# Performance work log

Measured on AMD Instinct MI355X. Metric: run time of the kernel, lower is better.

Reference implementation:

```python
import jax, jax.numpy as jnp
import numpy as np

N = 100000      # nodes on each bipartite side
E = 1600000     # edges
D_IN = 128      # input feature dim
H, C = 2, 50    # heads, per-head out channels
B = 64          # graphs in batch
NEG_SLOPE = 0.2 # GATConv leaky_relu slope


def setup_inputs() -> dict:
    key = jax.random.key(0)
    ks = jax.random.split(key, 12)
    glorot = lambda k, shape: (jax.random.uniform(k, shape, jnp.float32, -1.0, 1.0)
                               * jnp.sqrt(6.0 / (shape[0] + shape[-1])))
    return {
        "x_s": jax.random.normal(ks[0], (N, D_IN), jnp.float32),
        "x_t": jax.random.normal(ks[1], (N, D_IN), jnp.float32),
        "edge_index": jax.random.randint(ks[2], (2, E), 0, N, jnp.int64),
        "distances": jax.random.uniform(ks[3], (E,), jnp.float32),
        "x_s_batch": jnp.sort(jax.random.randint(ks[4], (N,), 0, B, jnp.int64)),
        "x_t_batch": jnp.sort(jax.random.randint(ks[5], (N,), 0, B, jnp.int64)),
        "W_src": glorot(ks[6], (D_IN, H * C)),
        "W_dst": glorot(ks[7], (D_IN, H * C)),
        "att_src": glorot(ks[8], (H, C)),
        "att_dst": glorot(ks[9], (H, C)),
        "bias_conv": jnp.zeros((H * C,), jnp.float32),
        "fc_w": glorot(ks[10], (H * C, 1)),
        "fc_b": jnp.zeros((1,), jnp.float32),
    }


def reference(x_s, x_t, edge_index, distances, x_s_batch, x_t_batch,
              W_src, W_dst, att_src, att_dst, bias_conv, fc_w, fc_b):
    src, dst = edge_index[0], edge_index[1]
    # Bipartite GATConv (edge_attr ignored: built with edge_dim=None)
    hs = (x_s @ W_src).reshape(N, H, C)            # [N,H,C]
    ht = (x_t @ W_dst).reshape(N, H, C)
    a_src = jnp.einsum('nhc,hc->nh', hs, att_src)  # [N,H]
    a_dst = jnp.einsum('nhc,hc->nh', ht, att_dst)
    e = jax.nn.leaky_relu(a_src[src] + a_dst[dst], NEG_SLOPE)   # [E,H]
    # segment softmax over edges sharing a target node
    m = jax.ops.segment_max(e, dst, num_segments=N)             # [N,H]
    ex = jnp.exp(e - m[dst])
    denom = jax.ops.segment_sum(ex, dst, num_segments=N)
    alpha = ex / (denom[dst] + 1e-16)                           # [E,H]
    # scatter-aggregate weighted source messages
    msg = alpha[:, :, None] * hs[src]                           # [E,H,C]
    out = jax.ops.segment_sum(msg, dst, num_segments=N)         # [N,H,C]
    out = out.reshape(N, H * C) + bias_conv
    x = jax.nn.relu(out)
    # global mean pool (original uses x_s_batch)
    pooled = jax.ops.segment_sum(x, x_s_batch, num_segments=B)
    counts = jax.ops.segment_sum(jnp.ones((N,), x.dtype), x_s_batch, num_segments=B)
    pooled = pooled / jnp.maximum(counts, 1.0)[:, None]         # [B,H*C]
    y = pooled @ fc_w + fc_b                                    # [B,1]
    return y.squeeze(-1)
```

## Files before the change

kernel.cpp:

```cpp
#include <hip/hip_runtime.h>
#include <math.h>

#define D_IN 128
#define HC 100
#define PW 128
#define CAP 64
#define NEG 0.2f
#define BINSH 8
#define NBIN 391
#define BCAP 4608
#define ACH 4096
#define YSLOT 32

typedef __attribute__((ext_vector_type(8))) short short8;
typedef __attribute__((ext_vector_type(4))) float f32x4;
typedef __attribute__((ext_vector_type(2))) float f32x2;

__device__ __forceinline__ float lrelu(float x){ return x > 0.f ? x : NEG*x; }

__device__ __forceinline__ unsigned short f2bf(float f){
  union { float f; unsigned u; } v; v.f = f;
  unsigned r = v.u + 0x7fffu + ((v.u >> 16) & 1u);
  return (unsigned short)(r >> 16);
}
__device__ __forceinline__ float bflo(unsigned u){
  union { unsigned x; float f; } v; v.x = u << 16; return v.f;
}
__device__ __forceinline__ float bfhi(unsigned u){
  union { unsigned x; float f; } v; v.x = u & 0xffff0000u; return v.f;
}

__global__ __launch_bounds__(256) void k_init(const float* __restrict__ Wd,
    const float* __restrict__ attd, const float* __restrict__ Ws,
    const float* __restrict__ bias, const float* __restrict__ fcw,
    const float* __restrict__ fcb, const int* __restrict__ xsb,
    float* __restrict__ wv, float* __restrict__ bias_p, float* __restrict__ fcwp,
    unsigned short* __restrict__ Wp, float* __restrict__ invb,
    int* __restrict__ bincnt, float* __restrict__ ypart,
    float* __restrict__ y, int N, int B){
  __shared__ int lo[257];
  int t = threadIdx.x;
  if (blockIdx.x == 0){
    int h = t >> 7, k = t & 127;
    float s = 0.f;
    #pragma unroll
    for (int c = 0; c < 50; ++c) s += Wd[k*HC + h*50 + c] * attd[h*50 + c];
    wv[t] = s;
    if (t < 128){
      bool cv = (t < 50) || (t >= 56 && t < 106);
      int c = (t < 50) ? t : t - 6;
      bias_p[t] = cv ? bias[c] : 0.f;
      fcwp[t]   = cv ? fcw[c]  : 0.f;
    }
    if (t < B) y[t] = fcb[0];
    bincnt[t] = 0; bincnt[t + 256] = 0;
    if (t <= B && t < 257){
      int key = t, l = 0, hi = N;
      while (l < hi){ int mid = (l+hi)>>1; if (xsb[mid] < key) l = mid+1; else hi = mid; }
      lo[t] = l;
    }
    __syncthreads();
    if (t < B){
      int c = lo[t+1] - lo[t];
      invb[t] = 1.f / (float)((c > 0) ? c : 1);
    }
  } else if (blockIdx.x == 1){
    for (int idx = t; idx < 1792; idx += 256){
      int ct = idx >> 8, kk = (idx >> 6) & 3, lane = idx & 63;
      int kb = kk*32 + (lane >> 4)*8;
      int c  = ct*16 + (lane & 15);
      #pragma unroll
      for (int j = 0; j < 8; ++j){
        float v = (c < HC) ? Ws[(size_t)(kb + j)*HC + c] : 0.f;
        Wp[idx*8 + j] = f2bf(v);
      }
    }
  } else {
    float4 z = make_float4(0.f,0.f,0.f,0.f);
    float4* yp4 = (float4*)ypart + (size_t)(blockIdx.x - 2)*8192;
    for (int i = t; i < 8192; i += 256) yp4[i] = z;
  }
}

__global__ __launch_bounds__(256) void k_fused(
    const float* __restrict__ x_s, const unsigned short* __restrict__ Wp,
    const float* __restrict__ atts, unsigned short* __restrict__ hsb,
    float* __restrict__ a_src,
    const float* __restrict__ x_t, const float* __restrict__ wv,
    float* __restrict__ a_dst,
    const int* __restrict__ ei, int* __restrict__ bincnt,
    int2* __restrict__ ebuf,
    int N, int E, int Gg, int Ga)
{
  __shared__ __align__(16) unsigned char smem[16384];
  int t = threadIdx.x;
  int bid = blockIdx.x;

  if (bid < Gg){
    unsigned short* hls = (unsigned short*)smem;
    int lane = t & 63, w = t >> 6;
    int qr = lane & 15, qq = lane >> 4;
    int row0 = bid*64;

    for (int i = t; i < 4096; i += 256) ((unsigned*)hls)[i] = 0u;

    int arow = row0 + w*16 + qr;
    bool rv = arow < N;
    short8 afr[4];
    const float* xp = x_s + (size_t)arow*D_IN + qq*8;
    #pragma unroll
    for (int kk = 0; kk < 4; ++kk){
      float4 v0 = make_float4(0.f,0.f,0.f,0.f), v1 = v0;
      if (rv){ v0 = *(const float4*)(xp + kk*32); v1 = *(const float4*)(xp + kk*32 + 4); }
      short8 a;
      a[0]=(short)f2bf(v0.x); a[1]=(short)f2bf(v0.y); a[2]=(short)f2bf(v0.z); a[3]=(short)f2bf(v0.w);
      a[4]=(short)f2bf(v1.x); a[5]=(short)f2bf(v1.y); a[6]=(short)f2bf(v1.z); a[7]=(short)f2bf(v1.w);
      afr[kk] = a;
    }

    f32x4 acc[7];
    #pragma unroll
    for (int ct = 0; ct < 7; ++ct) acc[ct] = (f32x4){0.f,0.f,0.f,0.f};
    #pragma unroll
    for (int kk = 0; kk < 4; ++kk){
      #pragma unroll
      for (int ct = 0; ct < 7; ++ct){
        short8 b = *(const short8*)&Wp[(size_t)((ct*4+kk)*64 + lane)*8];
        acc[ct] = __builtin_amdgcn_mfma_f32_16x16x32_bf16(afr[kk], b, acc[ct], 0, 0, 0);
      }
    }

    float p0[4] = {0,0,0,0}, p1[4] = {0,0,0,0};
    #pragma unroll
    for (int ct = 0; ct < 7; ++ct){
      int c = ct*16 + qr;
      if (c < HC){
        float av = atts[c];
        #pragma unroll
        for (int r = 0; r < 4; ++r){
          float v = acc[ct][r];
          if (c < 50) p0[r] += v*av; else p1[r] += v*av;
        }
      }
    }
    #pragma unroll
    for (int d = 1; d < 16; d <<= 1){
      #pragma unroll
      for (int r = 0; r < 4; ++r){
        p0[r] += __shfl_xor(p0[r], d, 64);
        p1[r] += __shfl_xor(p1[r], d, 64);
      }
    }
    if (qr == 0){
      #pragma unroll
      for (int r = 0; r < 4; ++r){
        int row = row0 + w*16 + qq*4 + r;
        if (row < N){ a_src[row*2] = p0[r]; a_src[row*2+1] = p1[r]; }
      }
    }

    __syncthreads();
    #pragma unroll
    for (int ct = 0; ct < 7; ++ct){
      int c = ct*16 + qr;
      if (c < HC){
        int p = (c < 50) ? c : c + 6;
        #pragma unroll
        for (int r = 0; r < 4; ++r)
          hls[(w*16 + qq*4 + r)*PW + p] = f2bf(acc[ct][r]);
      }
    }
    __syncthreads();
    unsigned* hg = (unsigned*)(hsb + (size_t)row0*PW);
    for (int i = t; i < 4096; i += 256) hg[i] = ((unsigned*)hls)[i];

  } else if (bid < Gg + Ga){
    float* wsh = (float*)smem;
    wsh[t] = wv[t];
    __syncthreads();
    int lane = t & 63;
    int n = (bid - Gg)*4 + (t >> 6);
    if (n >= N) return;
    float2 x2 = *(const float2*)&x_t[(size_t)n*D_IN + lane*2];
    float p0 = x2.x*wsh[lane*2]       + x2.y*wsh[lane*2+1];
    float p1 = x2.x*wsh[128+lane*2]   + x2.y*wsh[128+lane*2+1];
    #pragma unroll
    for (int d = 32; d >= 1; d >>= 1){ p0 += __shfl_xor(p0,d,64); p1 += __shfl_xor(p1,d,64); }
    if (lane == 0){ a_dst[n*2] = p0; a_dst[n*2+1] = p1; }

  } else {
    int* cnt   = (int*)smem;
    int* gbase = (int*)smem + 512;
    int e0 = (bid - Gg - Ga) * ACH;
    cnt[t] = 0; cnt[t + 256] = 0;
    __syncthreads();

    int src[16], dst[16], rank[16];
    #pragma unroll
    for (int j = 0; j < 4; ++j){
      int e = e0 + t*16 + j*4;
      bool in = (e + 4 <= E);
      int4 s4 = in ? *(const int4*)&ei[e]     : make_int4(0,0,0,0);
      int4 d4 = in ? *(const int4*)&ei[E + e] : make_int4(-1,-1,-1,-1);
      src[j*4+0]=s4.x; src[j*4+1]=s4.y; src[j*4+2]=s4.z; src[j*4+3]=s4.w;
      dst[j*4+0]=d4.x; dst[j*4+1]=d4.y; dst[j*4+2]=d4.z; dst[j*4+3]=d4.w;
    }
    #pragma unroll
    for (int j = 0; j < 16; ++j)
      rank[j] = (dst[j] >= 0) ? atomicAdd(&cnt[dst[j] >> BINSH], 1) : -1;
    __syncthreads();
    for (int i = t; i < NBIN; i += 256)
      gbase[i] = (cnt[i] > 0) ? atomicAdd(&bincnt[i], cnt[i]) : 0;
    __syncthreads();
    #pragma unroll
    for (int j = 0; j < 16; ++j){
      if (rank[j] >= 0){
        int b = dst[j] >> BINSH;
        int gp = gbase[b] + rank[j];
        if (gp < BCAP) ebuf[(size_t)b*BCAP + gp] = make_int2(src[j], dst[j]);
      }
    }
  }
}

__global__ __launch_bounds__(1024) void k_binB(const int* __restrict__ bincnt,
    const int2* __restrict__ ebuf, int* __restrict__ cur, int* __restrict__ csrc, int N)
{
  __shared__ int cnt2[256];
  int t = threadIdx.x, b = blockIdx.x;
  if (t < 256) cnt2[t] = 0;
  __syncthreads();
  int nE = bincnt[b]; if (nE > BCAP) nE = BCAP;
  const int2* eb = ebuf + (size_t)b*BCAP;
  for (int i = t; i < nE; i += 1024){
    int2 sd = eb[i];
    int ld = sd.y & 255;
    int p = atomicAdd(&cnt2[ld], 1);
    if (p < CAP) csrc[(size_t)sd.y*CAP + p] = sd.x;
  }
  __syncthreads();
  int n = b*256 + t;
  if (t < 256 && n < N) cur[n] = cnt2[t];
}

__global__ __launch_bounds__(256) void k_agg(const int* __restrict__ cur,
    const int* __restrict__ csrc, const float* __restrict__ a_src,
    const float* __restrict__ a_dst, const unsigned short* __restrict__ hsb,
    const float* __restrict__ bias_p, const float* __restrict__ fcwp,
    const int* __restrict__ xsb, float* __restrict__ ypart, int N)
{
  int t = threadIdx.x;
  int lane = t & 63;
  int w = t >> 6;
  int n = blockIdx.x*4 + w;
  if (n >= N) return;

  int deg = cur[n]; if (deg > CAP) deg = CAP;
  size_t o = (size_t)n * CAP;
  float2 ad = *(const float2*)&a_dst[n*2];

  int sreg = (lane < deg) ? csrc[o + lane] : 0;

  int k = lane & 15, g = lane >> 4;
  bool actv = (k < 14);
  bool hsel = (k >= 7);

#define PREF(vv, e) { int s_ = __shfl(sreg, (e), 64); \
    vv = (actv && (e) < deg) ? *(const uint4*)&hsb[(size_t)s_*PW + k*8] \
                             : make_uint4(0u,0u,0u,0u); }

  uint4 v0, v1, v2, v3;
  PREF(v0, g) PREF(v1, 4+g) PREF(v2, 8+g) PREF(v3, 12+g)

  float e0 = -INFINITY, e1 = -INFINITY;
  if (lane < deg){
    float2 as = *(const float2*)&a_src[sreg*2];
    e0 = lrelu(as.x + ad.x);
    e1 = lrelu(as.y + ad.y);
  }
  float m0 = e0, m1 = e1;
  if (deg > 32){ m0 = fmaxf(m0, __shfl_xor(m0,32,64)); m1 = fmaxf(m1, __shfl_xor(m1,32,64)); }
  if (deg > 16){ m0 = fmaxf(m0, __shfl_xor(m0,16,64)); m1 = fmaxf(m1, __shfl_xor(m1,16,64)); }
  #pragma unroll
  for (int d = 8; d >= 1; d >>= 1){
    m0 = fmaxf(m0, __shfl_xor(m0,d,64)); m1 = fmaxf(m1, __shfl_xor(m1,d,64));
  }
  float x0 = 0.f, x1 = 0.f;
  if (lane < deg){ x0 = __expf(e0 - m0); x1 = __expf(e1 - m1); }
  float d0 = x0, d1 = x1;
  if (deg > 32){ d0 += __shfl_xor(d0,32,64); d1 += __shfl_xor(d1,32,64); }
  if (deg > 16){ d0 += __shfl_xor(d0,16,64); d1 += __shfl_xor(d1,16,64); }
  #pragma unroll
  for (int d = 8; d >= 1; d >>= 1){ d0 += __shfl_xor(d0,d,64); d1 += __shfl_xor(d1,d,64); }
  float inv0 = __builtin_amdgcn_rcpf(d0 + 1e-16f);
  float inv1 = __builtin_amdgcn_rcpf(d1 + 1e-16f);
  float al0 = x0 * inv0, al1 = x1 * inv1;

#define CONS(vv, e) { float a0_ = __shfl(al0, (e), 64); float a1_ = __shfl(al1, (e), 64); \
    float a_ = hsel ? a1_ : a0_; f32x2 av_ = {a_, a_}; \
    f32x2 h0_ = {bflo(vv.x), bfhi(vv.x)}; acc0 += av_*h0_; \
    f32x2 h1_ = {bflo(vv.y), bfhi(vv.y)}; acc1 += av_*h1_; \
    f32x2 h2_ = {bflo(vv.z), bfhi(vv.z)}; acc2 += av_*h2_; \
    f32x2 h3_ = {bflo(vv.w), bfhi(vv.w)}; acc3 += av_*h3_; }

  f32x2 acc0 = {0.f,0.f}, acc1 = {0.f,0.f}, acc2 = {0.f,0.f}, acc3 = {0.f,0.f};
  int base = 0;
  for (;;){
    CONS(v0, base+g);
    if (base + 4 >= deg) break;
    CONS(v1, base+4+g);
    if (base + 8 >= deg) break;
    CONS(v2, base+8+g);
    if (base + 12 >= deg) break;
    CONS(v3, base+12+g);
    base += 16;
    if (base >= deg) break;
    PREF(v0, base+g) PREF(v1, base+4+g) PREF(v2, base+8+g) PREF(v3, base+12+g)
  }

  float acc[8] = {acc0.x, acc0.y, acc1.x, acc1.y, acc2.x, acc2.y, acc3.x, acc3.y};
  #pragma unroll
  for (int j = 0; j < 8; ++j){
    acc[j] += __shfl_xor(acc[j], 16, 64);
    acc[j] += __shfl_xor(acc[j], 32, 64);
  }

  float s = 0.f;
  if (g == 0 && actv){
    float4 b0 = *(const float4*)&bias_p[k*8];
    float4 b1 = *(const float4*)&bias_p[k*8 + 4];
    float4 f0 = *(const float4*)&fcwp[k*8];
    float4 f1 = *(const float4*)&fcwp[k*8 + 4];
    s  = fmaxf(acc[0]+b0.x, 0.f)*f0.x + fmaxf(acc[1]+b0.y, 0.f)*f0.y
       + fmaxf(acc[2]+b0.z, 0.f)*f0.z + fmaxf(acc[3]+b0.w, 0.f)*f0.w
       + fmaxf(acc[4]+b1.x, 0.f)*f1.x + fmaxf(acc[5]+b1.y, 0.f)*f1.y
       + fmaxf(acc[6]+b1.z, 0.f)*f1.z + fmaxf(acc[7]+b1.w, 0.f)*f1.w;
  }
  #pragma unroll
  for (int d = 1; d <= 8; d <<= 1) s += __shfl_xor(s, d, 64);
  if (lane == 0){
    int b = xsb[n];
    atomicAdd(&ypart[(size_t)((b*YSLOT + (blockIdx.x & (YSLOT-1))) << 5)], s);
  }
#undef PREF
#undef CONS
}

__global__ __launch_bounds__(64) void k_red(const float* __restrict__ ypart,
    const float* __restrict__ invb, float* __restrict__ y)
{
  int b = blockIdx.x, t = threadIdx.x;
  float v = (t < YSLOT) ? ypart[(size_t)((b*YSLOT + t) << 5)] : 0.f;
  #pragma unroll
  for (int d = 16; d >= 1; d >>= 1) v += __shfl_xor(v, d, 64);
  if (t == 0) y[b] += v * invb[b];
}

extern "C" void kernel_launch(void* const* d_in, const int* in_sizes, int n_in,
                              void* d_out, int out_size, void* d_ws, size_t ws_size,
                              hipStream_t stream)
{
  const float* x_s  = (const float*)d_in[0];
  const float* x_t  = (const float*)d_in[1];
  const int*   ei   = (const int*)d_in[2];
  const int*   xsb  = (const int*)d_in[4];
  const float* Ws   = (const float*)d_in[6];
  const float* Wd   = (const float*)d_in[7];
  const float* atts = (const float*)d_in[8];
  const float* attd = (const float*)d_in[9];
  const float* bias = (const float*)d_in[10];
  const float* fcw  = (const float*)d_in[11];
  const float* fcb  = (const float*)d_in[12];
  float* y = (float*)d_out;

  const int N = in_sizes[4];
  const int E = in_sizes[3];
  const int B = out_size;

  char* p = (char*)d_ws;
  auto carve = [&](size_t bytes)->char*{
    char* r = p; p += (bytes + 255) & ~(size_t)255; return r;
  };
  int*            cur    = (int*)           carve((size_t)N*4);
  int*            csrc   = (int*)           carve((size_t)N*CAP*4);
  float*          wv     = (float*)         carve(256*4);
  float*          a_src  = (float*)         carve((size_t)N*2*4);
  float*          a_dst  = (float*)         carve((size_t)N*2*4);
  unsigned short* hsb    = (unsigned short*)carve((size_t)(N+64)*PW*2);
  float*          bias_p = (float*)         carve(128*4);
  float*          fcwp   = (float*)         carve(128*4);
  unsigned short* Wp     = (unsigned short*)carve((size_t)1792*8*2);
  float*          invb   = (float*)         carve(256*4);
  int*            bincnt = (int*)           carve(512*4);
  float*          ypart  = (float*)         carve((size_t)B*YSLOT*32*4);
  int2*           ebuf   = (int2*)          carve((size_t)NBIN*BCAP*8);

  const int Gg = (N + 63) / 64;
  const int Ga = (N + 3) / 4;
  const int Gb = (E + ACH - 1) / ACH;

  k_init  <<<4, 256, 0, stream>>>(Wd, attd, Ws, bias, fcw, fcb, xsb,
                                  wv, bias_p, fcwp, Wp, invb, bincnt, ypart, y, N, B);
  k_fused <<<Gg + Ga + Gb, 256, 0, stream>>>(x_s, Wp, atts, hsb, a_src,
                                             x_t, wv, a_dst,
                                             ei, bincnt, ebuf, N, E, Gg, Ga);
  k_binB  <<<NBIN, 1024, 0, stream>>>(bincnt, ebuf, cur, csrc, N);
  k_agg   <<<(N+3)/4, 256, 0, stream>>>(cur, csrc, a_src, a_dst, hsb,
                                        bias_p, fcwp, xsb, ypart, N);
  k_red   <<<B, 64, 0, stream>>>(ypart, invb, y);
}
```

Before: 314.2 us.

## Fuse bin-to-CSR build into aggregation kernel and merge a_dst into GEMM blocks

Removes the separate k_binB pass and the global csrc/cur arrays. Each aggregation block now takes one bin of 128 destination nodes, builds per-node source lists in shared memory, and processes 16 nodes per wave. The a_dst projection is also folded into the GEMM blocks, which already cover the same rows, so the separate attention-dst blocks are gone. Bins are halved (BINSH 7, NBIN 782). This cuts global traffic and one launch, at the cost of fewer, larger agg blocks (782 blocks of 512 threads, 32KB of LDS each), which may reduce occupancy and load balance.

```diff
diff --git a/kernel.cpp b/kernel.cpp
--- a/kernel.cpp
+++ b/kernel.cpp
@@ -6,9 +6,9 @@
 #define PW 128
 #define CAP 64
 #define NEG 0.2f
-#define BINSH 8
-#define NBIN 391
-#define BCAP 4608
+#define BINSH 7
+#define NBIN 782
+#define BCAP 2432
 #define ACH 4096
 #define YSLOT 32
 
@@ -53,7 +53,7 @@
       fcwp[t]   = cv ? fcw[c]  : 0.f;
     }
     if (t < B) y[t] = fcb[0];
-    bincnt[t] = 0; bincnt[t + 256] = 0;
+    for (int i = t; i < NBIN; i += 256) bincnt[i] = 0;
     if (t <= B && t < 257){
       int key = t, l = 0, hi = N;
       while (l < hi){ int mid = (l+hi)>>1; if (xsb[mid] < key) l = mid+1; else hi = mid; }
@@ -90,18 +90,20 @@
     float* __restrict__ a_dst,
     const int* __restrict__ ei, int* __restrict__ bincnt,
     int2* __restrict__ ebuf,
-    int N, int E, int Gg, int Ga)
+    int N, int E, int Gg)
 {
-  __shared__ __align__(16) unsigned char smem[16384];
+  __shared__ __align__(16) unsigned char smem[17408];
   int t = threadIdx.x;
   int bid = blockIdx.x;
 
   if (bid < Gg){
     unsigned short* hls = (unsigned short*)smem;
+    float* wsh = (float*)(smem + 16384);
     int lane = t & 63, w = t >> 6;
     int qr = lane & 15, qq = lane >> 4;
     int row0 = bid*64;
 
+    wsh[t] = wv[t];
     for (int i = t; i < 4096; i += 256) ((unsigned*)hls)[i] = 0u;
 
     int arow = row0 + w*16 + qr;
@@ -117,6 +119,24 @@
       a[4]=(short)f2bf(v1.x); a[5]=(short)f2bf(v1.y); a[6]=(short)f2bf(v1.z); a[7]=(short)f2bf(v1.w);
       afr[kk] = a;
     }
+
+    __syncthreads();
+
+    float pd0 = 0.f, pd1 = 0.f;
+    const float* xtp = x_t + (size_t)arow*D_IN + qq*8;
+    #pragma unroll
+    for (int kk = 0; kk < 4; ++kk){
+      float4 u0 = make_float4(0.f,0.f,0.f,0.f), u1 = u0;
+      if (rv){ u0 = *(const float4*)(xtp + kk*32); u1 = *(const float4*)(xtp + kk*32 + 4); }
+      int kb = qq*8 + kk*32;
+      pd0 += u0.x*wsh[kb+0] + u0.y*wsh[kb+1] + u0.z*wsh[kb+2] + u0.w*wsh[kb+3]
+           + u1.x*wsh[kb+4] + u1.y*wsh[kb+5] + u1.z*wsh[kb+6] + u1.w*wsh[kb+7];
+      pd1 += u0.x*wsh[128+kb+0] + u0.y*wsh[128+kb+1] + u0.z*wsh[128+kb+2] + u0.w*wsh[128+kb+3]
+           + u1.x*wsh[128+kb+4] + u1.y*wsh[128+kb+5] + u1.z*wsh[128+kb+6] + u1.w*wsh[128+kb+7];
+    }
+    pd0 += __shfl_xor(pd0, 16, 64); pd0 += __shfl_xor(pd0, 32, 64);
+    pd1 += __shfl_xor(pd1, 16, 64); pd1 += __shfl_xor(pd1, 32, 64);
+    if (qq == 0 && rv){ a_dst[arow*2] = pd0; a_dst[arow*2+1] = pd1; }
 
     f32x4 acc[7];
     #pragma unroll
@@ -159,7 +179,6 @@
       }
     }
 
-    __syncthreads();
     #pragma unroll
     for (int ct = 0; ct < 7; ++ct){
       int c = ct*16 + qr;
@@ -174,25 +193,11 @@
     unsigned* hg = (unsigned*)(hsb + (size_t)row0*PW);
     for (int i = t; i < 4096; i += 256) hg[i] = ((unsigned*)hls)[i];
 
-  } else if (bid < Gg + Ga){
-    float* wsh = (float*)smem;
-    wsh[t] = wv[t];
-    __syncthreads();
-    int lane = t & 63;
-    int n = (bid - Gg)*4 + (t >> 6);
-    if (n >= N) return;
-    float2 x2 = *(const float2*)&x_t[(size_t)n*D_IN + lane*2];
-    float p0 = x2.x*wsh[lane*2]       + x2.y*wsh[lane*2+1];
-    float p1 = x2.x*wsh[128+lane*2]   + x2.y*wsh[128+lane*2+1];
-    #pragma unroll
-    for (int d = 32; d >= 1; d >>= 1){ p0 += __shfl_xor(p0,d,64); p1 += __shfl_xor(p1,d,64); }
-    if (lane == 0){ a_dst[n*2] = p0; a_dst[n*2+1] = p1; }
-
   } else {
     int* cnt   = (int*)smem;
-    int* gbase = (int*)smem + 512;
-    int e0 = (bid - Gg - Ga) * ACH;
-    cnt[t] = 0; cnt[t + 256] = 0;
+    int* gbase = (int*)smem + NBIN;
+    int e0 = (bid - Gg) * ACH;
+    for (int i = t; i < NBIN; i += 256) cnt[i] = 0;
     __syncthreads();
 
     int src[16], dst[16], rank[16];
@@ -223,44 +228,28 @@
   }
 }
 
-__global__ __launch_bounds__(1024) void k_binB(const int* __restrict__ bincnt,
-    const int2* __restrict__ ebuf, int* __restrict__ cur, int* __restrict__ csrc, int N)
-{
-  __shared__ int cnt2[256];
-  int t = threadIdx.x, b = blockIdx.x;
-  if (t < 256) cnt2[t] = 0;
-  __syncthreads();
-  int nE = bincnt[b]; if (nE > BCAP) nE = BCAP;
-  const int2* eb = ebuf + (size_t)b*BCAP;
-  for (int i = t; i < nE; i += 1024){
-    int2 sd = eb[i];
-    int ld = sd.y & 255;
-    int p = atomicAdd(&cnt2[ld], 1);
-    if (p < CAP) csrc[(size_t)sd.y*CAP + p] = sd.x;
-  }
-  __syncthreads();
-  int n = b*256 + t;
-  if (t < 256 && n < N) cur[n] = cnt2[t];
-}
-
-__global__ __launch_bounds__(256) void k_agg(const int* __restrict__ cur,
-    const int* __restrict__ csrc, const float* __restrict__ a_src,
+__global__ __launch_bounds__(512) void k_agg(const int* __restrict__ bincnt,
+    const int2* __restrict__ ebuf, const float* __restrict__ a_src,
     const float* __restrict__ a_dst, const unsigned short* __restrict__ hsb,
     const float* __restrict__ bias_p, const float* __restrict__ fcwp,
     const int* __restrict__ xsb, float* __restrict__ ypart, int N)
 {
-  int t = threadIdx.x;
-  int lane = t & 63;
-  int w = t >> 6;
-  int n = blockIdx.x*4 + w;
-  if (n >= N) return;
-
-  int deg = cur[n]; if (deg > CAP) deg = CAP;
-  size_t o = (size_t)n * CAP;
-  float2 ad = *(const float2*)&a_dst[n*2];
-
-  int sreg = (lane < deg) ? csrc[o + lane] : 0;
-
+  __shared__ int lsrc[128*CAP];
+  __shared__ int lcnt[128];
+  int t = threadIdx.x, b = blockIdx.x;
+  if (t < 128) lcnt[t] = 0;
+  __syncthreads();
+  int nE = bincnt[b]; if (nE > BCAP) nE = BCAP;
+  const int2* eb = ebuf + (size_t)b*BCAP;
+  for (int i = t; i < nE; i += 512){
+    int2 sd = eb[i];
+    int ld = sd.y & 127;
+    int p = atomicAdd(&lcnt[ld], 1);
+    if (p < CAP) lsrc[ld*CAP + p] = sd.x;
+  }
+  __syncthreads();
+
+  int lane = t & 63, w = t >> 6;
   int k = lane & 15, g = lane >> 4;
   bool actv = (k < 14);
   bool hsel = (k >= 7);
@@ -268,33 +257,6 @@
 #define PREF(vv, e) { int s_ = __shfl(sreg, (e), 64); \
     vv = (actv && (e) < deg) ? *(const uint4*)&hsb[(size_t)s_*PW + k*8] \
                              : make_uint4(0u,0u,0u,0u); }
-
-  uint4 v0, v1, v2, v3;
-  PREF(v0, g) PREF(v1, 4+g) PREF(v2, 8+g) PREF(v3, 12+g)
-
-  float e0 = -INFINITY, e1 = -INFINITY;
-  if (lane < deg){
-    float2 as = *(const float2*)&a_src[sreg*2];
-    e0 = lrelu(as.x + ad.x);
-    e1 = lrelu(as.y + ad.y);
-  }
-  float m0 = e0, m1 = e1;
-  if (deg > 32){ m0 = fmaxf(m0, __shfl_xor(m0,32,64)); m1 = fmaxf(m1, __shfl_xor(m1,32,64)); }
-  if (deg > 16){ m0 = fmaxf(m0, __shfl_xor(m0,16,64)); m1 = fmaxf(m1, __shfl_xor(m1,16,64)); }
-  #pragma unroll
-  for (int d = 8; d >= 1; d >>= 1){
-    m0 = fmaxf(m0, __shfl_xor(m0,d,64)); m1 = fmaxf(m1, __shfl_xor(m1,d,64));
-  }
-  float x0 = 0.f, x1 = 0.f;
-  if (lane < deg){ x0 = __expf(e0 - m0); x1 = __expf(e1 - m1); }
-  float d0 = x0, d1 = x1;
-  if (deg > 32){ d0 += __shfl_xor(d0,32,64); d1 += __shfl_xor(d1,32,64); }
-  if (deg > 16){ d0 += __shfl_xor(d0,16,64); d1 += __shfl_xor(d1,16,64); }
-  #pragma unroll
-  for (int d = 8; d >= 1; d >>= 1){ d0 += __shfl_xor(d0,d,64); d1 += __shfl_xor(d1,d,64); }
-  float inv0 = __builtin_amdgcn_rcpf(d0 + 1e-16f);
-  float inv1 = __builtin_amdgcn_rcpf(d1 + 1e-16f);
-  float al0 = x0 * inv0, al1 = x1 * inv1;
 
 #define CONS(vv, e) { float a0_ = __shfl(al0, (e), 64); float a1_ = __shfl(al1, (e), 64); \
     float a_ = hsel ? a1_ : a0_; f32x2 av_ = {a_, a_}; \
@@ -303,44 +265,80 @@
     f32x2 h2_ = {bflo(vv.z), bfhi(vv.z)}; acc2 += av_*h2_; \
     f32x2 h3_ = {bflo(vv.w), bfhi(vv.w)}; acc3 += av_*h3_; }
 
-  f32x2 acc0 = {0.f,0.f}, acc1 = {0.f,0.f}, acc2 = {0.f,0.f}, acc3 = {0.f,0.f};
-  int base = 0;
-  for (;;){
-    CONS(v0, base+g);
-    if (base + 4 >= deg) break;
-    CONS(v1, base+4+g);
-    if (base + 8 >= deg) break;
-    CONS(v2, base+8+g);
-    if (base + 12 >= deg) break;
-    CONS(v3, base+12+g);
-    base += 16;
-    if (base >= deg) break;
-    PREF(v0, base+g) PREF(v1, base+4+g) PREF(v2, base+8+g) PREF(v3, base+12+g)
-  }
-
-  float acc[8] = {acc0.x, acc0.y, acc1.x, acc1.y, acc2.x, acc2.y, acc3.x, acc3.y};
-  #pragma unroll
-  for (int j = 0; j < 8; ++j){
-    acc[j] += __shfl_xor(acc[j], 16, 64);
-    acc[j] += __shfl_xor(acc[j], 32, 64);
-  }
-
-  float s = 0.f;
-  if (g == 0 && actv){
-    float4 b0 = *(const float4*)&bias_p[k*8];
-    float4 b1 = *(const float4*)&bias_p[k*8 + 4];
-    float4 f0 = *(const float4*)&fcwp[k*8];
-    float4 f1 = *(const float4*)&fcwp[k*8 + 4];
-    s  = fmaxf(acc[0]+b0.x, 0.f)*f0.x + fmaxf(acc[1]+b0.y, 0.f)*f0.y
-       + fmaxf(acc[2]+b0.z, 0.f)*f0.z + fmaxf(acc[3]+b0.w, 0.f)*f0.w
-       + fmaxf(acc[4]+b1.x, 0.f)*f1.x + fmaxf(acc[5]+b1.y, 0.f)*f1.y
-       + fmaxf(acc[6]+b1.z, 0.f)*f1.z + fmaxf(acc[7]+b1.w, 0.f)*f1.w;
-  }
-  #pragma unroll
-  for (int d = 1; d <= 8; d <<= 1) s += __shfl_xor(s, d, 64);
-  if (lane == 0){
-    int b = xsb[n];
-    atomicAdd(&ypart[(size_t)((b*YSLOT + (blockIdx.x & (YSLOT-1))) << 5)], s);
+  for (int it = 0; it < 16; ++it){
+    int nl = w*16 + it;
+    int n  = b*128 + nl;
+    if (n >= N) break;
+    int deg = lcnt[nl]; if (deg > CAP) deg = CAP;
+    float2 ad = *(const float2*)&a_dst[n*2];
+    int sreg = (lane < deg) ? lsrc[nl*CAP + lane] : 0;
+
+    uint4 v0, v1, v2, v3;
+    PREF(v0, g) PREF(v1, 4+g) PREF(v2, 8+g) PREF(v3, 12+g)
+
+    float e0 = -INFINITY, e1 = -INFINITY;
+    if (lane < deg){
+      float2 as = *(const float2*)&a_src[sreg*2];
+      e0 = lrelu(as.x + ad.x);
+      e1 = lrelu(as.y + ad.y);
+    }
+    float m0 = e0, m1 = e1;
+    if (deg > 32){ m0 = fmaxf(m0, __shfl_xor(m0,32,64)); m1 = fmaxf(m1, __shfl_xor(m1,32,64)); }
+    if (deg > 16){ m0 = fmaxf(m0, __shfl_xor(m0,16,64)); m1 = fmaxf(m1, __shfl_xor(m1,16,64)); }
+    #pragma unroll
+    for (int d = 8; d >= 1; d >>= 1){
+      m0 = fmaxf(m0, __shfl_xor(m0,d,64)); m1 = fmaxf(m1, __shfl_xor(m1,d,64));
+    }
+    float x0 = 0.f, x1 = 0.f;
+    if (lane < deg){ x0 = __expf(e0 - m0); x1 = __expf(e1 - m1); }
+    float d0 = x0, d1 = x1;
+    if (deg > 32){ d0 += __shfl_xor(d0,32,64); d1 += __shfl_xor(d1,32,64); }
+    if (deg > 16){ d0 += __shfl_xor(d0,16,64); d1 += __shfl_xor(d1,16,64); }
+    #pragma unroll
+    for (int d = 8; d >= 1; d >>= 1){ d0 += __shfl_xor(d0,d,64); d1 += __shfl_xor(d1,d,64); }
+    float inv0 = __builtin_amdgcn_rcpf(d0 + 1e-16f);
+    float inv1 = __builtin_amdgcn_rcpf(d1 + 1e-16f);
+    float al0 = x0 * inv0, al1 = x1 * inv1;
+
+    f32x2 acc0 = {0.f,0.f}, acc1 = {0.f,0.f}, acc2 = {0.f,0.f}, acc3 = {0.f,0.f};
+    int base = 0;
+    for (;;){
+      CONS(v0, base+g);
+      if (base + 4 >= deg) break;
+      CONS(v1, base+4+g);
+      if (base + 8 >= deg) break;
+      CONS(v2, base+8+g);
+      if (base + 12 >= deg) break;
+      CONS(v3, base+12+g);
+      base += 16;
+      if (base >= deg) break;
+      PREF(v0, base+g) PREF(v1, base+4+g) PREF(v2, base+8+g) PREF(v3, base+12+g)
+    }
+
+    float acc[8] = {acc0.x, acc0.y, acc1.x, acc1.y, acc2.x, acc2.y, acc3.x, acc3.y};
+    #pragma unroll
+    for (int j = 0; j < 8; ++j){
+      acc[j] += __shfl_xor(acc[j], 16, 64);
+      acc[j] += __shfl_xor(acc[j], 32, 64);
+    }
+
+    float s = 0.f;
+    if (g == 0 && actv){
+      float4 b0 = *(const float4*)&bias_p[k*8];
+      float4 b1 = *(const float4*)&bias_p[k*8 + 4];
+      float4 f0 = *(const float4*)&fcwp[k*8];
+      float4 f1 = *(const float4*)&fcwp[k*8 + 4];
+      s  = fmaxf(acc[0]+b0.x, 0.f)*f0.x + fmaxf(acc[1]+b0.y, 0.f)*f0.y
+         + fmaxf(acc[2]+b0.z, 0.f)*f0.z + fmaxf(acc[3]+b0.w, 0.f)*f0.w
+         + fmaxf(acc[4]+b1.x, 0.f)*f1.x + fmaxf(acc[5]+b1.y, 0.f)*f1.y
+         + fmaxf(acc[6]+b1.z, 0.f)*f1.z + fmaxf(acc[7]+b1.w, 0.f)*f1.w;
+    }
+    #pragma unroll
+    for (int d = 1; d <= 8; d <<= 1) s += __shfl_xor(s, d, 64);
+    if (lane == 0){
+      int bb = xsb[n];
+      atomicAdd(&ypart[(size_t)((bb*YSLOT + (b & (YSLOT-1))) << 5)], s);
+    }
   }
 #undef PREF
 #undef CONS
@@ -381,8 +379,6 @@
   auto carve = [&](size_t bytes)->char*{
     char* r = p; p += (bytes + 255) & ~(size_t)255; return r;
   };
-  int*            cur    = (int*)           carve((size_t)N*4);
-  int*            csrc   = (int*)           carve((size_t)N*CAP*4);
   float*          wv     = (float*)         carve(256*4);
   float*          a_src  = (float*)         carve((size_t)N*2*4);
   float*          a_dst  = (float*)         carve((size_t)N*2*4);
@@ -391,21 +387,19 @@
   float*          fcwp   = (float*)         carve(128*4);
   unsigned short* Wp     = (unsigned short*)carve((size_t)1792*8*2);
   float*          invb   = (float*)         carve(256*4);
-  int*            bincnt = (int*)           carve(512*4);
+  int*            bincnt = (int*)           carve(1024*4);
   float*          ypart  = (float*)         carve((size_t)B*YSLOT*32*4);
   int2*           ebuf   = (int2*)          carve((size_t)NBIN*BCAP*8);
 
   const int Gg = (N + 63) / 64;
-  const int Ga = (N + 3) / 4;
   const int Gb = (E + ACH - 1) / ACH;
 
   k_init  <<<4, 256, 0, stream>>>(Wd, attd, Ws, bias, fcw, fcb, xsb,
                                   wv, bias_p, fcwp, Wp, invb, bincnt, ypart, y, N, B);
-  k_fused <<<Gg + Ga + Gb, 256, 0, stream>>>(x_s, Wp, atts, hsb, a_src,
-                                             x_t, wv, a_dst,
-                                             ei, bincnt, ebuf, N, E, Gg, Ga);
-  k_binB  <<<NBIN, 1024, 0, stream>>>(bincnt, ebuf, cur, csrc, N);
-  k_agg   <<<(N+3)/4, 256, 0, stream>>>(cur, csrc, a_src, a_dst, hsb,
-                                        bias_p, fcwp, xsb, ypart, N);
+  k_fused <<<Gg + Gb, 256, 0, stream>>>(x_s, Wp, atts, hsb, a_src,
+                                        x_t, wv, a_dst,
+                                        ei, bincnt, ebuf, N, E, Gg);
+  k_agg   <<<NBIN, 512, 0, stream>>>(bincnt, ebuf, a_src, a_dst, hsb,
+                                     bias_p, fcwp, xsb, ypart, N);
   k_red   <<<B, 64, 0, stream>>>(ypart, invb, y);
 }
```

Measured after the change: 313.0 us. No clear change (-0.4%).
